# Performance work log

Hardware: AMD Instinct MI355X
Metric: run time of the kernel (lower is better)

Reference implementation:

```python
import jax, jax.numpy as jnp
import numpy as np

SIGMA = 1.0
LN2 = 0.6931471805599453


def _raster_mask(kd, kh, kw, include_center):
    # PixelCNN-style causal mask in (depth, h, w) raster order
    idx = np.arange(kd * kh * kw).reshape(kd, kh, kw)
    c = (kd * kh * kw) // 2
    m = (idx <= c) if include_center else (idx < c)
    return jnp.asarray(m, jnp.float32)[None, None]  # [1,1,kd,kh,kw] (OIDHW broadcast)


def _conv3d(x, w, b, padding):
    y = jax.lax.conv_general_dilated(x, w, (1, 1, 1), padding,
                                     dimension_numbers=('NCDHW', 'OIDHW', 'NCDHW'))
    return y + b[None, :, None, None, None]


def _quantize1d(x, centers):
    # distances of every element to every center: [..., L]
    d = (x[..., None] - centers) ** 2
    phi_soft = jax.nn.softmax(-SIGMA * d, axis=-1)
    qsoft = jnp.einsum('...l,l->...', phi_soft, centers)
    symbols = jnp.argmin(d, axis=-1)  # int32 hard assignment
    qhard = centers[symbols]
    return qsoft, qhard, symbols


def setup_inputs() -> dict:
    key = jax.random.key(0)
    ks = jax.random.split(key, 8)
    N, H, W, C = 4, 128, 128, 16
    K, L = 24, 6
    s = 0.05
    return {
        'x': jax.random.normal(ks[0], (N, H, W, C), jnp.float32),
        'centers': jax.random.uniform(ks[1], (L,), jnp.float32, -2.0, 2.0),
        'w0': jax.random.normal(ks[2], (K, 1, 3, 3, 3), jnp.float32) * s,
        'b0': jnp.zeros((K,), jnp.float32),
        'w1': jax.random.normal(ks[3], (K, K, 3, 3, 3), jnp.float32) * s,
        'b1': jnp.zeros((K,), jnp.float32),
        'w2': jax.random.normal(ks[4], (K, K, 3, 3, 3), jnp.float32) * s,
        'b2': jnp.zeros((K,), jnp.float32),
        'w_out': jax.random.normal(ks[5], (L, K, 1, 1, 1), jnp.float32) * s,
        'b_out': jnp.zeros((L,), jnp.float32),
    }


def reference(x, centers, w0, b0, w1, b1, w2, b2, w_out, b_out):
    # ---- soft/hard quantization with straight-through estimator ----
    qsoft, qhard, symbols = _quantize1d(x, centers)
    qbar = qsoft + jax.lax.stop_gradient(qhard - qsoft)  # [N,H,W,C] NHWC

    pc_in = jnp.transpose(qbar, (0, 3, 1, 2))[:, None]      # [N,1,C,H,W] (depth=C)
    tgt = jnp.transpose(symbols, (0, 3, 1, 2))              # [N,C,H,W]

    # pad input volume with pad_value = centers[0] (causal boundary symbol)
    pad_value = centers[0].astype(pc_in.dtype)
    v = jax.lax.pad(pc_in, pad_value,
                    [(0, 0, 0), (0, 0, 0), (1, 1, 0), (1, 1, 0), (1, 1, 0)])

    mask_a = _raster_mask(3, 3, 3, include_center=False)
    mask_b = _raster_mask(3, 3, 3, include_center=True)

    # res_shallow: masked-A conv -> masked-B conv -> masked-B conv + residual -> 1x1x1 logits
    h0 = jax.nn.relu(_conv3d(v, w0 * mask_a, b0, 'VALID'))     # [N,K,C,H,W]
    h1 = jax.nn.relu(_conv3d(h0, w1 * mask_b, b1, 'SAME'))
    h2 = _conv3d(h1, w2 * mask_b, b2, 'SAME') + h0
    logits = _conv3d(jax.nn.relu(h2), w_out, b_out, 'SAME')    # [N,L,C,H,W]

    # per-element bitcost: cross-entropy of hard symbols, in bits
    lp = jax.nn.log_softmax(logits, axis=1)
    bc = -jnp.take_along_axis(lp, tgt[:, None], axis=1)[:, 0] / LN2  # [N,C,H,W]
    bc_train = jnp.transpose(bc, (0, 2, 3, 1))                        # NCHW -> NHWC
    return qbar, bc_train
```

## Files before the change

### kernel.cpp

```cpp
#include <hip/hip_runtime.h>
#include <cstddef>

typedef _Float16 f16;
typedef _Float16 f16x8 __attribute__((ext_vector_type(8)));
typedef float f32x16 __attribute__((ext_vector_type(16)));

#define N_ 4
#define D_ 16
#define H_ 128
#define W_ 128
#define K_ 24
#define L_ 6
#define NTAP_A 13

#define OFF_TGT  0ull
#define OFF_Q16  4194304ull
#define OFF_H0   6291456ull
#define OFF_H1   56623104ull
#define OFF_W0P  106954752ull
#define OFF_W1B  106956800ull
#define OFF_W2B  106978304ull

#define AROW_B 6336
#define A_BYTES 120384
#define B_BYTES 21504
#define SMEM_BYTES 141888

__host__ __device__ constexpr int aoff(int p, int c, int g) {
  int idx8 = 2 * c + g;
  int ts = idx8 >= 3 ? 1 : 0;
  int t = 2 * p + ts;
  int cb = idx8 - 3 * ts;
  int dz = t / 9 - 1;
  int rr = t % 9;
  int dy = rr / 3 - 1;
  int dx = rr % 3 - 1;
  int rowb = (dz < 0) ? (dy + 1) : (10 + dy + 1);
  return rowb * AROW_B + (dx + 1) * 48 + cb * 16;
}

__device__ __forceinline__ void quant1(float xv, const float cs[L_],
                                       float& qb, int& sym) {
  float dv[L_];
  float dmin = 3.4e38f;
  sym = 0;
#pragma unroll
  for (int l = 0; l < L_; ++l) {
    float df = xv - cs[l];
    float d = df * df;
    dv[l] = d;
    if (d < dmin) { dmin = d; sym = l; }
  }
  float e[L_];
  float s = 0.f;
#pragma unroll
  for (int l = 0; l < L_; ++l) {
    e[l] = expf(dmin - dv[l]);
    s += e[l];
  }
  float qsoft = 0.f;
#pragma unroll
  for (int l = 0; l < L_; ++l) qsoft += (e[l] / s) * cs[l];
  qb = qsoft + (cs[sym] - qsoft);
}

__global__ __launch_bounds__(256) void quant_all_k(
    const float* __restrict__ x, const float* __restrict__ centers,
    float* __restrict__ qbar_out, f16* __restrict__ q16,
    int* __restrict__ tgt,
    const float* __restrict__ w0, const float* __restrict__ w1,
    const float* __restrict__ w2, float* __restrict__ w0p,
    f16* __restrict__ w1B, f16* __restrict__ w2B) {
  __shared__ f16 q16s[2048];
  __shared__ int syms[2048];

  int blk = blockIdx.x;
  int n = blk >> 7;
  int h = blk & 127;
  int t = threadIdx.x;

  float cs[L_];
#pragma unroll
  for (int l = 0; l < L_; ++l) cs[l] = centers[l];

  const float4* x4 = (const float4*)x + (size_t)blk * 512;
  float4* o4 = (float4*)qbar_out + (size_t)blk * 512;

  int w = t >> 1;
  int c0 = (t & 1) * 8;
#pragma unroll
  for (int e = 0; e < 2; ++e) {
    float4 v = x4[2 * t + e];
    float4 o;
    float qb; int sym;
    quant1(v.x, cs, qb, sym); o.x = qb;
    q16s[(c0 + 4 * e + 0) * 128 + w] = (f16)qb; syms[(c0 + 4 * e + 0) * 128 + w] = sym;
    quant1(v.y, cs, qb, sym); o.y = qb;
    q16s[(c0 + 4 * e + 1) * 128 + w] = (f16)qb; syms[(c0 + 4 * e + 1) * 128 + w] = sym;
    quant1(v.z, cs, qb, sym); o.z = qb;
    q16s[(c0 + 4 * e + 2) * 128 + w] = (f16)qb; syms[(c0 + 4 * e + 2) * 128 + w] = sym;
    quant1(v.w, cs, qb, sym); o.w = qb;
    q16s[(c0 + 4 * e + 3) * 128 + w] = (f16)qb; syms[(c0 + 4 * e + 3) * 128 + w] = sym;
    o4[2 * t + e] = o;
  }
  __syncthreads();

  for (int i = t; i < 2048; i += 256) {
    int dd = i >> 7, ww = i & 127;
    size_t g = ((size_t)(n * D_ + dd) * H_ + h) * W_ + ww;
    q16[g] = q16s[i];
    tgt[g] = syms[i];
  }

  int pid = blk * 256 + t;
  if (pid < NTAP_A * K_) {
    int co = pid % K_;
    int tt = pid / K_;
    w0p[tt * K_ + co] = w0[co * 27 + tt];
  } else if (pid < NTAP_A * K_ + 2 * 10752) {
    int i2 = pid - NTAP_A * K_;
    int sel = i2 / 10752;
    int idx2 = i2 % 10752;
    int chunk = idx2 / 512;
    int r = idx2 % 512;
    int g = r / 256;
    int nn = (r % 256) / 8;
    int j = r % 8;
    int p = chunk / 3, cc = chunk % 3;
    int idx8 = 2 * cc + g;
    int ts = idx8 >= 3 ? 1 : 0;
    int tp = 2 * p + ts;
    int ci = (idx8 - 3 * ts) * 8 + j;
    const float* wsrc = sel ? w2 : w1;
    float v = (nn < K_) ? wsrc[(nn * K_ + ci) * 27 + tp] : 0.f;
    (sel ? w2B : w1B)[idx2] = (f16)v;
  }
}

__global__ __launch_bounds__(256) void conv0_q16_k(
    const f16* __restrict__ q16, const float* __restrict__ centers,
    const float* __restrict__ w0p, const float* __restrict__ b0,
    f16* __restrict__ h0) {
  __shared__ f16 qs[2 * 6 * 132];

  int blk = blockIdx.x;
  int hb = blk & 31;
  int d = (blk >> 5) & 15;
  int n = blk >> 9;
  int h_base = hb * 4;

  f16 pv16 = (f16)centers[0];

  for (int i = threadIdx.x; i < 1584; i += 256) {
    int pl = i / 792;
    int rr = (i / 132) % 6;
    int s = i % 132;
    int qp = d - 1 + pl;
    int hh = h_base - 1 + rr;
    int ww = s - 1;
    f16 val = pv16;
    if (qp >= 0 && (unsigned)hh < (unsigned)H_ && (unsigned)ww < (unsigned)W_)
      val = q16[((size_t)(n * D_ + qp) * H_ + hh) * W_ + ww];
    qs[i] = val;
  }
  __syncthreads();

  float bia[K_];
#pragma unroll
  for (int co = 0; co < K_; ++co) bia[co] = b0[co];

#pragma unroll
  for (int k2 = 0; k2 < 2; ++k2) {
    int pos = threadIdx.x + 256 * k2;
    int rl = pos >> 7;
    int w = pos & 127;

    float acc[K_];
#pragma unroll
    for (int co = 0; co < K_; ++co) acc[co] = bia[co];

#pragma unroll
    for (int t = 0; t < NTAP_A; ++t) {
      int dz, dy, dx;
      if (t < 9)       { dz = -1; dy = t / 3 - 1; dx = t % 3 - 1; }
      else if (t < 12) { dz = 0;  dy = -1;        dx = t - 10; }
      else             { dz = 0;  dy = 0;         dx = -1; }
      float qv = (float)qs[(dz + 1) * 792 + (rl + dy + 1) * 132 + (w + dx + 1)];
      const float* wr = w0p + t * K_;
#pragma unroll
      for (int co = 0; co < K_; ++co) acc[co] = fmaf(qv, wr[co], acc[co]);
    }

    union { f16 hv[K_]; uint4 u[3]; } u;
#pragma unroll
    for (int co = 0; co < K_; ++co) u.hv[co] = (f16)fmaxf(acc[co], 0.f);
    uint4* dst = (uint4*)(h0 + ((size_t)((n * D_ + d) * H_ + h_base + rl) * W_ + w) * K_);
    dst[0] = u.u[0]; dst[1] = u.u[1]; dst[2] = u.u[2];
  }
}

__device__ __forceinline__ void conv_core8(const f16* __restrict__ src,
                                           const f16* __restrict__ wB,
                                           char* smem, int n, int d, int h_base,
                                           f32x16& acc0, f32x16& acc1) {
  const int tid = threadIdx.x;
  for (int i = tid; i < 7296; i += 1024) {
    int r = i / 384, qq = i % 384;
    int dd = (r < 10) ? d - 1 : d;
    int hh = h_base - 1 + ((r < 10) ? r : r - 10);
    uint4 v = make_uint4(0, 0, 0, 0);
    if (dd >= 0 && (unsigned)hh < (unsigned)H_)
      v = ((const uint4*)(src + (size_t)((n * D_ + dd) * H_ + hh) * 3072))[qq];
    *(uint4*)(smem + r * AROW_B + 48 + qq * 16) = v;
  }
  if (tid < 114) {
    int r = tid / 6, k = tid % 6;
    int byte = r * AROW_B + (k < 3 ? k * 16 : 6192 + (k - 3) * 16);
    *(uint4*)(smem + byte) = make_uint4(0, 0, 0, 0);
  }
  {
    const uint4* g = (const uint4*)wB;
    uint4* s = (uint4*)(smem + A_BYTES);
    for (int i = tid; i < 1344; i += 1024) s[i] = g[i];
  }
  __syncthreads();

  const int lane = tid & 63;
  const int wv = tid >> 6;
  const int m = lane & 31;
  const int g01 = lane >> 5;

  const int hs = wv >> 1;
  const int wc0 = (wv & 1) * 64;
  const char* Ab0 = smem + hs * AROW_B + (wc0 + m) * 48;
  const char* Ab1 = Ab0 + 32 * 48;
  const char* Bb = smem + A_BYTES + g01 * 512 + m * 16;

#pragma unroll
  for (int r = 0; r < 16; ++r) { acc0[r] = 0.f; acc1[r] = 0.f; }

#pragma unroll
  for (int p = 0; p < 7; ++p) {
#pragma unroll
    for (int c = 0; c < 3; ++c) {
      const int C0 = aoff(p, c, 0);
      const int C1 = aoff(p, c, 1);
      int off = g01 ? C1 : C0;
      f16x8 b = *(const f16x8*)(Bb + (p * 3 + c) * 1024);
      f16x8 a0 = *(const f16x8*)(Ab0 + off);
      f16x8 a1 = *(const f16x8*)(Ab1 + off);
      acc0 = __builtin_amdgcn_mfma_f32_32x32x16_f16(a0, b, acc0, 0, 0, 0);
      acc1 = __builtin_amdgcn_mfma_f32_32x32x16_f16(a1, b, acc1, 0, 0, 0);
    }
  }
}

__global__ __launch_bounds__(1024, 1) void conv1_mfma_k(
    const f16* __restrict__ src, const f16* __restrict__ wB,
    const float* __restrict__ bias, f16* __restrict__ dst) {
  __shared__ __align__(16) char smem[SMEM_BYTES];

  int blk = blockIdx.x;
  int hb = blk & 15;
  int d = (blk >> 4) & 15;
  int n = blk >> 8;
  int h_base = hb * 8;

  f32x16 acc0, acc1;
  conv_core8(src, wB, smem, n, d, h_base, acc0, acc1);

  const int lane = threadIdx.x & 63;
  const int wv = threadIdx.x >> 6;
  const int m = lane & 31;
  const int g01 = lane >> 5;

  __syncthreads();
  f16* ldsE = (f16*)smem;
  if (m < K_) {
    float bv = bias[m];
#pragma unroll
    for (int tt = 0; tt < 2; ++tt) {
      const f32x16& A = tt ? acc1 : acc0;
#pragma unroll
      for (int r = 0; r < 16; ++r) {
        int mrow = (r & 3) + 8 * (r >> 2) + 4 * g01;
        int pos = (2 * wv + tt) * 32 + mrow;
        ldsE[pos * K_ + m] = (f16)fmaxf(A[r] + bv, 0.f);
      }
    }
  }
  __syncthreads();
  {
    uint4* g = (uint4*)(dst + (size_t)((n * D_ + d) * H_ + h_base) * 3072);
    const uint4* s = (const uint4*)smem;
    for (int i = threadIdx.x; i < 3072; i += 1024) g[i] = s[i];
  }
}

__global__ __launch_bounds__(1024, 1) void conv2_mfma_k(
    const f16* __restrict__ h1, const f16* __restrict__ h0,
    const f16* __restrict__ wB, const float* __restrict__ bias,
    const float* __restrict__ w_out, const float* __restrict__ b_out,
    const int* __restrict__ tgt, float* __restrict__ bco) {
  __shared__ __align__(16) char smem[SMEM_BYTES];

  int blk = blockIdx.x;
  int hb = blk & 15;
  int d = (blk >> 4) & 15;
  int n = blk >> 8;
  int h_base = hb * 8;

  f32x16 acc0, acc1;
  conv_core8(h1, wB, smem, n, d, h_base, acc0, acc1);

  const int lane = threadIdx.x & 63;
  const int wv = threadIdx.x >> 6;
  const int m = lane & 31;
  const int g01 = lane >> 5;

  __syncthreads();
  float* Ef = (float*)smem;
  if (m < K_) {
    float bv = bias[m];
#pragma unroll
    for (int tt = 0; tt < 2; ++tt) {
      const f32x16& A = tt ? acc1 : acc0;
#pragma unroll
      for (int r = 0; r < 16; ++r) {
        int mrow = (r & 3) + 8 * (r >> 2) + 4 * g01;
        int pos = (2 * wv + tt) * 32 + mrow;
        Ef[pos * 28 + m] = A[r] + bv;
      }
    }
  }
  __syncthreads();

  {
    int pos = threadIdx.x;
    int hh = h_base + (pos >> 7);
    int w = pos & 127;

    size_t gpos = (size_t)((n * D_ + d) * H_ + h_base) * W_ + pos;
    const f16x8* hp = (const f16x8*)(h0 + gpos * K_);
    f16x8 e0 = hp[0], e1 = hp[1], e2 = hp[2];

    const float* ef = Ef + pos * 28;
    float vals[K_];
#pragma unroll
    for (int k = 0; k < K_; ++k) {
      float h0v = (float)(k < 8 ? e0[k] : (k < 16 ? e1[k - 8] : e2[k - 16]));
      vals[k] = fmaxf(ef[k] + h0v, 0.f);
    }

    float lg[L_];
#pragma unroll
    for (int l = 0; l < L_; ++l) lg[l] = b_out[l];
#pragma unroll
    for (int k = 0; k < K_; ++k) {
      float rv = vals[k];
#pragma unroll
      for (int l = 0; l < L_; ++l) lg[l] = fmaf(rv, w_out[l * K_ + k], lg[l]);
    }
    float mm = lg[0];
#pragma unroll
    for (int l = 1; l < L_; ++l) mm = fmaxf(mm, lg[l]);
    float s = 0.f;
#pragma unroll
    for (int l = 0; l < L_; ++l) s += expf(lg[l] - mm);

    int t = tgt[gpos];
    float lt = lg[0];
#pragma unroll
    for (int l = 1; l < L_; ++l) lt = (t == l) ? lg[l] : lt;

    float lp = lt - mm - logf(s);
    bco[(size_t)((n * H_ + hh) * W_ + w) * D_ + d] = -lp / 0.69314718055994530942f;
  }
}

extern "C" void kernel_launch(void* const* d_in, const int* in_sizes, int n_in,
                              void* d_out, int out_size, void* d_ws, size_t ws_size,
                              hipStream_t stream) {
  const float* x       = (const float*)d_in[0];
  const float* centers = (const float*)d_in[1];
  const float* w0      = (const float*)d_in[2];
  const float* b0      = (const float*)d_in[3];
  const float* w1      = (const float*)d_in[4];
  const float* b1      = (const float*)d_in[5];
  const float* w2      = (const float*)d_in[6];
  const float* b2      = (const float*)d_in[7];
  const float* w_out   = (const float*)d_in[8];
  const float* b_out   = (const float*)d_in[9];
  float* out = (float*)d_out;

  char* ws = (char*)d_ws;
  int*   tg   = (int*)(ws + OFF_TGT);
  f16*   q16  = (f16*)(ws + OFF_Q16);
  f16*   h0f  = (f16*)(ws + OFF_H0);
  f16*   h1f  = (f16*)(ws + OFF_H1);
  float* w0p  = (float*)(ws + OFF_W0P);
  f16*   w1B  = (f16*)(ws + OFF_W1B);
  f16*   w2B  = (f16*)(ws + OFF_W2B);

  hipLaunchKernelGGL(quant_all_k, dim3(512), dim3(256), 0, stream,
                     x, centers, out, q16, tg, w0, w1, w2, w0p, w1B, w2B);
  hipLaunchKernelGGL(conv0_q16_k, dim3(2048), dim3(256), 0, stream,
                     q16, centers, w0p, b0, h0f);
  hipLaunchKernelGGL(conv1_mfma_k, dim3(1024), dim3(1024), 0, stream,
                     h0f, w1B, b1, h1f);
  hipLaunchKernelGGL(conv2_mfma_k, dim3(1024), dim3(1024), 0, stream,
                     h1f, h0f, w2B, b2, w_out, b_out, tg, out + 1048576);
}
```

Before: 200.6 us.

## Store activations channel-group-planar to remove LDS bank conflicts in MFMA conv

Changes the h0/h1 global layout from interleaved 24-channel-per-pixel to three planes of 8 channels each. The LDS staging tile changes to match, so each lane's A-fragment reads become 16-byte strided instead of 48-byte strided. This is meant to reduce LDS bank conflicts in the MFMA inner loop and keep global reads coalesced. It touches the conv0 writer, the conv1/conv2 tile loaders, the epilogue and the residual read, which adds index arithmetic and some risk of layout mismatch.

```diff
diff --git a/kernel.cpp b/kernel.cpp
--- a/kernel.cpp
+++ b/kernel.cpp
@@ -13,6 +13,8 @@
 #define L_ 6
 #define NTAP_A 13
 
+#define PLANE_H 131072
+
 #define OFF_TGT  0ull
 #define OFF_Q16  4194304ull
 #define OFF_H0   6291456ull
@@ -21,10 +23,12 @@
 #define OFF_W1B  106956800ull
 #define OFF_W2B  106978304ull
 
-#define AROW_B 6336
+#define APL_B  40128
+#define AR_B   2112
 #define A_BYTES 120384
 #define B_BYTES 21504
 #define SMEM_BYTES 141888
+#define EPL_B 16416
 
 __host__ __device__ constexpr int aoff(int p, int c, int g) {
   int idx8 = 2 * c + g;
@@ -36,7 +40,7 @@
   int dy = rr / 3 - 1;
   int dx = rr % 3 - 1;
   int rowb = (dz < 0) ? (dy + 1) : (10 + dy + 1);
-  return rowb * AROW_B + (dx + 1) * 48 + cb * 16;
+  return cb * APL_B + rowb * AR_B + (dx + 1) * 16;
 }
 
 __device__ __forceinline__ void quant1(float xv, const float cs[L_],
@@ -169,6 +173,8 @@
 #pragma unroll
   for (int co = 0; co < K_; ++co) bia[co] = b0[co];
 
+  f16* nd = h0 + (size_t)(n * D_ + d) * (3 * PLANE_H);
+
 #pragma unroll
   for (int k2 = 0; k2 < 2; ++k2) {
     int pos = threadIdx.x + 256 * k2;
@@ -191,11 +197,13 @@
       for (int co = 0; co < K_; ++co) acc[co] = fmaf(qv, wr[co], acc[co]);
     }
 
-    union { f16 hv[K_]; uint4 u[3]; } u;
-#pragma unroll
-    for (int co = 0; co < K_; ++co) u.hv[co] = (f16)fmaxf(acc[co], 0.f);
-    uint4* dst = (uint4*)(h0 + ((size_t)((n * D_ + d) * H_ + h_base + rl) * W_ + w) * K_);
-    dst[0] = u.u[0]; dst[1] = u.u[1]; dst[2] = u.u[2];
+#pragma unroll
+    for (int g = 0; g < 3; ++g) {
+      union { f16 hv[8]; uint4 u; } u;
+#pragma unroll
+      for (int j = 0; j < 8; ++j) u.hv[j] = (f16)fmaxf(acc[g * 8 + j], 0.f);
+      *(uint4*)(nd + g * PLANE_H + (size_t)(h_base + rl) * (W_ * 8) + w * 8) = u.u;
+    }
   }
 }
 
@@ -205,23 +213,27 @@
                                            f32x16& acc0, f32x16& acc1) {
   const int tid = threadIdx.x;
   for (int i = tid; i < 7296; i += 1024) {
-    int r = i / 384, qq = i % 384;
+    int s = i & 127;
+    int rg = i >> 7;
+    int r = rg / 3, g = rg % 3;
     int dd = (r < 10) ? d - 1 : d;
     int hh = h_base - 1 + ((r < 10) ? r : r - 10);
     uint4 v = make_uint4(0, 0, 0, 0);
     if (dd >= 0 && (unsigned)hh < (unsigned)H_)
-      v = ((const uint4*)(src + (size_t)((n * D_ + dd) * H_ + hh) * 3072))[qq];
-    *(uint4*)(smem + r * AROW_B + 48 + qq * 16) = v;
+      v = *(const uint4*)(src + ((size_t)((n * D_ + dd) * 3 + g)) * PLANE_H +
+                          (size_t)hh * (W_ * 8) + s * 8);
+    *(uint4*)(smem + g * APL_B + r * AR_B + (s + 1) * 16) = v;
   }
   if (tid < 114) {
-    int r = tid / 6, k = tid % 6;
-    int byte = r * AROW_B + (k < 3 ? k * 16 : 6192 + (k - 3) * 16);
-    *(uint4*)(smem + byte) = make_uint4(0, 0, 0, 0);
+    int r = tid / 6, rem = tid % 6;
+    int g = rem >> 1, k = rem & 1;
+    *(uint4*)(smem + g * APL_B + r * AR_B + (k ? 129 : 0) * 16) =
+        make_uint4(0, 0, 0, 0);
   }
   {
-    const uint4* g = (const uint4*)wB;
+    const uint4* gsrc = (const uint4*)wB;
     uint4* s = (uint4*)(smem + A_BYTES);
-    for (int i = tid; i < 1344; i += 1024) s[i] = g[i];
+    for (int i = tid; i < 1344; i += 1024) s[i] = gsrc[i];
   }
   __syncthreads();
 
@@ -232,8 +244,8 @@
 
   const int hs = wv >> 1;
   const int wc0 = (wv & 1) * 64;
-  const char* Ab0 = smem + hs * AROW_B + (wc0 + m) * 48;
-  const char* Ab1 = Ab0 + 32 * 48;
+  const char* Ab0 = smem + hs * AR_B + (wc0 + m) * 16;
+  const char* Ab1 = Ab0 + 32 * 16;
   const char* Bb = smem + A_BYTES + g01 * 512 + m * 16;
 
 #pragma unroll
@@ -275,9 +287,9 @@
   const int g01 = lane >> 5;
 
   __syncthreads();
-  f16* ldsE = (f16*)smem;
   if (m < K_) {
     float bv = bias[m];
+    char* ep = smem + (m >> 3) * EPL_B + (m & 7) * 2;
 #pragma unroll
     for (int tt = 0; tt < 2; ++tt) {
       const f32x16& A = tt ? acc1 : acc0;
@@ -285,15 +297,18 @@
       for (int r = 0; r < 16; ++r) {
         int mrow = (r & 3) + 8 * (r >> 2) + 4 * g01;
         int pos = (2 * wv + tt) * 32 + mrow;
-        ldsE[pos * K_ + m] = (f16)fmaxf(A[r] + bv, 0.f);
+        *(f16*)(ep + pos * 16) = (f16)fmaxf(A[r] + bv, 0.f);
       }
     }
   }
   __syncthreads();
   {
-    uint4* g = (uint4*)(dst + (size_t)((n * D_ + d) * H_ + h_base) * 3072);
-    const uint4* s = (const uint4*)smem;
-    for (int i = threadIdx.x; i < 3072; i += 1024) g[i] = s[i];
+    f16* nd = dst + (size_t)(n * D_ + d) * (3 * PLANE_H) + (size_t)h_base * (W_ * 8);
+    for (int i = threadIdx.x; i < 3072; i += 1024) {
+      int g = i >> 10, j = i & 1023;
+      *(uint4*)(nd + g * PLANE_H + j * 8) =
+          *(const uint4*)(smem + g * EPL_B + j * 16);
+    }
   }
 }
 
@@ -340,9 +355,11 @@
     int hh = h_base + (pos >> 7);
     int w = pos & 127;
 
-    size_t gpos = (size_t)((n * D_ + d) * H_ + h_base) * W_ + pos;
-    const f16x8* hp = (const f16x8*)(h0 + gpos * K_);
-    f16x8 e0 = hp[0], e1 = hp[1], e2 = hp[2];
+    const f16* nd0 = h0 + (size_t)(n * D_ + d) * (3 * PLANE_H) +
+                     (size_t)h_base * (W_ * 8) + pos * 8;
+    f16x8 e0 = *(const f16x8*)(nd0);
+    f16x8 e1 = *(const f16x8*)(nd0 + PLANE_H);
+    f16x8 e2 = *(const f16x8*)(nd0 + 2 * PLANE_H);
 
     const float* ef = Ef + pos * 28;
     float vals[K_];
@@ -368,6 +385,7 @@
 #pragma unroll
     for (int l = 0; l < L_; ++l) s += expf(lg[l] - mm);
 
+    size_t gpos = (size_t)((n * D_ + d) * H_ + h_base) * W_ + pos;
     int t = tgt[gpos];
     float lt = lg[0];
 #pragma unroll
```

After: 203.0 us. Within noise of the previous version (+1.2%).
